# Optimization experiments

Measured on AMD Instinct MI355X. Metric: run time of the kernel, lower is better.

## Reference

```python
import jax, jax.numpy as jnp
import numpy as np

MARGIN = 0.3
EPS = 1e-6  # torch TripletMarginLoss pairwise_distance eps


def setup_inputs() -> dict:
    key = jax.random.key(0)
    k1, k2 = jax.random.split(key)
    n, d = 8192, 128
    inputs = jax.random.normal(k1, (n, d), dtype=jnp.float32)
    similarity = jax.random.randint(k2, (n, n), 0, 2, dtype=jnp.int32)
    return {"inputs": inputs, "similarity": similarity}


def reference(inputs, similarity):
    # mask[i, j] = True if j is a positive of anchor i
    mask = similarity != 0                      # (n, n) bool
    maskf = mask.astype(inputs.dtype)
    counts = maskf.sum(axis=1, keepdims=True)   # (n, 1), >0 by construction
    # per-anchor center = mean of its positives (masked mean as a GEMM)
    centers = (maskf @ inputs) / counts         # (n, d)
    # dist[i, j] = ||centers[i] - inputs[j]||_2 via the expansion trick
    # (avoids materializing the (n, n, d) difference tensor of the original)
    c2 = jnp.sum(centers * centers, axis=1)[:, None]
    x2 = jnp.sum(inputs * inputs, axis=1)[None, :]
    d2 = c2 + x2 - 2.0 * (centers @ inputs.T)
    dist = jnp.sqrt(jnp.maximum(d2, 0.0))       # (n, n)
    # dist only feeds argmin in the original (indices carry no grad)
    dist = jax.lax.stop_gradient(dist)
    # hard-negative mining: argmin of dist over negatives of each anchor
    neg_idx = jnp.argmin(jnp.where(mask, jnp.inf, dist), axis=1)  # (n,)
    neg_min = inputs[neg_idx]                   # (n, d)
    # TripletMarginLoss(margin=0.3, p=2): anchor=centers, pos=inputs, neg=neg_min
    d_ap = jnp.linalg.norm(centers - inputs + EPS, axis=1)
    d_an = jnp.linalg.norm(centers - neg_min + EPS, axis=1)
    return jnp.mean(jnp.maximum(d_ap - d_an + MARGIN, 0.0))
```

## Files before the change

kernel.cpp:

```cpp
#include <hip/hip_runtime.h>
#include <stdint.h>

#define NN 8192
#define DD 128

typedef float f32x4 __attribute__((ext_vector_type(4)));
typedef short bf16x8 __attribute__((ext_vector_type(8)));

union B8 { uint32_t u[4]; bf16x8 v; };

__device__ inline uint16_t f2bf(float f) {
  uint32_t u = __builtin_bit_cast(uint32_t, f);
  uint32_t r = (u + 0x7FFFu + ((u >> 16) & 1u)) >> 16;
  return (uint16_t)r;
}

__device__ inline f32x4 mfma16(bf16x8 a, bf16x8 b, f32x4 c) {
  return __builtin_amdgcn_mfma_f32_16x16x32_bf16(a, b, c, 0, 0, 0);
}

__global__ __launch_bounds__(256) void k_prep(const float* __restrict__ inp,
                                              uint16_t* __restrict__ inp_bf,
                                              uint16_t* __restrict__ inpT_bf,
                                              float* __restrict__ x2p,
                                              uint32_t* __restrict__ counts,
                                              uint32_t* __restrict__ negkey,
                                              float* __restrict__ out) {
  __shared__ uint16_t ldsT[128 * 65];
  __shared__ float ldsS[256];
  const int tid = threadIdx.x;
  const int gid = blockIdx.x * 256 + tid;
  if (gid < NN) { counts[gid] = 0u; negkey[gid] = 0xFFFFFFFFu; }
  if (gid == 0) out[0] = 0.f;
  const int j0 = blockIdx.x * 64;
  const int r = tid >> 2;
  const int dseg = (tid & 3) * 32;
  float ss = 0.f;
#pragma unroll
  for (int it = 0; it < 8; ++it) {
    float4 v = *(const float4*)(inp + (size_t)(j0 + r) * DD + dseg + it * 4);
    ss += v.x * v.x + v.y * v.y + v.z * v.z + v.w * v.w;
    uint16_t b0 = f2bf(v.x), b1 = f2bf(v.y), b2 = f2bf(v.z), b3 = f2bf(v.w);
    *(ushort4*)(inp_bf + (size_t)(j0 + r) * DD + dseg + it * 4) = make_ushort4(b0, b1, b2, b3);
    int d = dseg + it * 4;
    ldsT[(d + 0) * 65 + r] = b0;
    ldsT[(d + 1) * 65 + r] = b1;
    ldsT[(d + 2) * 65 + r] = b2;
    ldsT[(d + 3) * 65 + r] = b3;
  }
  ldsS[tid] = ss;
  __syncthreads();
  if (tid < 64)
    x2p[j0 + tid] = ldsS[tid * 4] + ldsS[tid * 4 + 1] + ldsS[tid * 4 + 2] + ldsS[tid * 4 + 3] + 512.0f;
#pragma unroll
  for (int it = 0; it < 32; ++it) {
    int flat = it * 256 + tid;
    int d = flat >> 6, jl = flat & 63;
    inpT_bf[(size_t)d * NN + j0 + jl] = ldsT[d * 65 + jl];
  }
}

__global__ __launch_bounds__(256, 2) void k_bitgen(const int* __restrict__ sim,
                                                   uint32_t* __restrict__ bmT,
                                                   uint32_t* __restrict__ counts) {
  __shared__ uint32_t ldsW[64 * 64];
  const int tid = threadIdx.x, lane = tid & 63, w = tid >> 6;
  const int m0 = blockIdx.x * 64;
  const int c0 = blockIdx.y * 2048;
  int va[32], vb[32];
  {
    const int* p = sim + (size_t)(m0 + w) * NN + c0 + lane;
#pragma unroll
    for (int s = 0; s < 32; ++s) va[s] = p[s * 64];
  }
#pragma unroll 1
  for (int rr = 0; rr < 16; ++rr) {
    const int rl = rr * 4 + w;
    if (rr < 15) {
      const int* p = sim + (size_t)(m0 + rl + 4) * NN + c0 + lane;
#pragma unroll
      for (int s = 0; s < 32; ++s) vb[s] = p[s * 64];
    }
    uint32_t cnt = 0;
#pragma unroll
    for (int s = 0; s < 32; ++s) {
      unsigned long long ball = __ballot(va[s] != 0);
      cnt += (uint32_t)__popcll(ball);
      if ((lane & 31) == 0)
        ldsW[(s * 2 + (lane >> 5)) * 64 + rl] = (uint32_t)(ball >> (lane & 32));
    }
    if (lane == 0) atomicAdd(&counts[m0 + rl], cnt);
#pragma unroll
    for (int s = 0; s < 32; ++s) va[s] = vb[s];
  }
  __syncthreads();
#pragma unroll
  for (int it = 0; it < 16; ++it) {
    int idx = it * 256 + tid;
    int kw = idx >> 6, r = idx & 63;
    bmT[(size_t)((c0 >> 5) + kw) * NN + m0 + r] = ldsW[idx];
  }
}

__global__ __launch_bounds__(256, 4) void k_gemm1(const uint16_t* __restrict__ inpT,
                                                  const uint32_t* __restrict__ bmT,
                                                  float* __restrict__ part) {
  __shared__ __align__(16) uint16_t ldsB[128 * 72];
  __shared__ uint32_t ldsM[128];
  const int tid = threadIdx.x, lane = tid & 63, w = tid >> 6;
  const int col = lane & 15, quad = lane >> 4;
  const int m0 = blockIdx.x * 64;
  const int kb0 = blockIdx.y * 1024;
  const int wm = (w >> 1) * 32, wn = (w & 1) * 64;
  const int dim = tid >> 1, koff = (tid & 1) * 32;
  const int mrow = tid >> 1, msel = tid & 1;
  f32x4 acc[2][4];
  const f32x4 z = {0.f, 0.f, 0.f, 0.f};
#pragma unroll
  for (int r = 0; r < 2; ++r)
#pragma unroll
    for (int c = 0; c < 4; ++c) acc[r][c] = z;

  bf16x8 bpf[4];
#pragma unroll
  for (int it = 0; it < 4; ++it)
    bpf[it] = *(const bf16x8*)(inpT + (size_t)dim * NN + kb0 + koff + it * 8);
  uint32_t mpf = (tid < 128) ? bmT[(size_t)((kb0 >> 5) + msel) * NN + m0 + mrow] : 0u;

  for (int ks = 0; ks < 16; ++ks) {
    const int kb = kb0 + ks * 64;
    __syncthreads();
#pragma unroll
    for (int it = 0; it < 4; ++it)
      *(bf16x8*)(ldsB + dim * 72 + koff + it * 8) = bpf[it];
    if (tid < 128) ldsM[mrow * 2 + msel] = mpf;
    __syncthreads();
    if (ks < 15) {
#pragma unroll
      for (int it = 0; it < 4; ++it)
        bpf[it] = *(const bf16x8*)(inpT + (size_t)dim * NN + kb + 64 + koff + it * 8);
      if (tid < 128) mpf = bmT[(size_t)(((kb + 64) >> 5) + msel) * NN + m0 + mrow];
    }
#pragma unroll
    for (int h = 0; h < 2; ++h) {
      B8 af[2];
#pragma unroll
      for (int rr = 0; rr < 2; ++rr) {
        uint32_t word = ldsM[(wm + rr * 16 + col) * 2 + h];
        uint32_t b = (word >> (quad * 8)) & 0xFFu;
        uint32_t s = b * 0x8001u;
#pragma unroll
        for (int p = 0; p < 4; ++p) {
          uint32_t t = (s >> (2 * p)) & 0x10001u;
          af[rr].u[p] = t * 0x3F80u;
        }
      }
#pragma unroll
      for (int cc = 0; cc < 4; ++cc) {
        bf16x8 bfr = *(const bf16x8*)(ldsB + (wn + cc * 16 + col) * 72 + h * 32 + quad * 8);
#pragma unroll
        for (int rr = 0; rr < 2; ++rr) acc[rr][cc] = mfma16(af[rr].v, bfr, acc[rr][cc]);
      }
    }
  }
  float* pp = part + (size_t)blockIdx.y * NN * DD;
#pragma unroll
  for (int rr = 0; rr < 2; ++rr)
#pragma unroll
    for (int cc = 0; cc < 4; ++cc)
#pragma unroll
      for (int g = 0; g < 4; ++g)
        pp[(size_t)(m0 + wm + rr * 16 + quad * 4 + g) * DD + wn + cc * 16 + col] = acc[rr][cc][g];
}

__global__ __launch_bounds__(256) void k_reduce(const float* __restrict__ part,
                                                const uint32_t* __restrict__ counts,
                                                float* __restrict__ centers,
                                                uint16_t* __restrict__ cen_bf) {
  const int gid = blockIdx.x * 256 + threadIdx.x;
  const int idx = gid * 4;
  const int row = idx >> 7;
  const float inv = 1.0f / (float)counts[row];
  float4 v = *(const float4*)(part + idx);
#pragma unroll
  for (int s = 1; s < 8; ++s) {
    float4 u = *(const float4*)(part + (size_t)s * NN * DD + idx);
    v.x += u.x; v.y += u.y; v.z += u.z; v.w += u.w;
  }
  v.x *= inv; v.y *= inv; v.z *= inv; v.w *= inv;
  *(float4*)(centers + idx) = v;
  *(ushort4*)(cen_bf + idx) = make_ushort4(f2bf(v.x), f2bf(v.y), f2bf(v.z), f2bf(v.w));
}

__global__ __launch_bounds__(256, 4) void k_argmin(const uint16_t* __restrict__ cen_bf,
                                                   const uint16_t* __restrict__ inp_bf,
                                                   const uint32_t* __restrict__ bmT,
                                                   const float* __restrict__ x2p,
                                                   uint32_t* __restrict__ negkey) {
  __shared__ __align__(16) uint16_t ldsB[64 * 136];
  __shared__ uint32_t ldsM[128];
  __shared__ float ldsX[64];
  __shared__ uint32_t ldsR[64];
  const int tid = threadIdx.x, lane = tid & 63, w = tid >> 6;
  const int col = lane & 15, quad = lane >> 4;
  const int i0 = blockIdx.x * 64;
  const int jbase = blockIdx.y * 1024;
  const int wi = (w >> 1) * 32, wj = (w & 1) * 32;
  bf16x8 af[2][4];
#pragma unroll
  for (int rr = 0; rr < 2; ++rr)
#pragma unroll
    for (int kk = 0; kk < 4; ++kk)
      af[rr][kk] = *(const bf16x8*)(cen_bf + (size_t)(i0 + wi + rr * 16 + col) * DD + kk * 32 + quad * 8);
  if (tid < 64) ldsR[tid] = 0xFFFFFFFFu;
  uint32_t best[2][4];
#pragma unroll
  for (int rr = 0; rr < 2; ++rr)
#pragma unroll
    for (int g = 0; g < 4; ++g) best[rr][g] = 0xFFFFFFFFu;

  const int jl = tid >> 2, doff = (tid & 3) * 32;
  bf16x8 bpf[4];
#pragma unroll
  for (int it = 0; it < 4; ++it)
    bpf[it] = *(const bf16x8*)(inp_bf + (size_t)(jbase + jl) * DD + doff + it * 8);
  uint32_t mpf = (tid < 128) ? bmT[(size_t)((jbase >> 5) + (tid >> 6)) * NN + i0 + (tid & 63)] : 0u;
  float xpf = (tid >= 128 && tid < 192) ? x2p[jbase + tid - 128] : 0.f;

  for (int js = 0; js < 16; ++js) {
    const int j0 = jbase + js * 64;
    __syncthreads();
#pragma unroll
    for (int it = 0; it < 4; ++it)
      *(bf16x8*)(ldsB + jl * 136 + doff + it * 8) = bpf[it];
    if (tid < 128) ldsM[tid] = mpf;
    else if (tid < 192) ldsX[tid - 128] = xpf;
    __syncthreads();
    if (js < 15) {
#pragma unroll
      for (int it = 0; it < 4; ++it)
        bpf[it] = *(const bf16x8*)(inp_bf + (size_t)(j0 + 64 + jl) * DD + doff + it * 8);
      if (tid < 128) mpf = bmT[(size_t)(((j0 + 64) >> 5) + (tid >> 6)) * NN + i0 + (tid & 63)];
      else if (tid < 192) xpf = x2p[j0 + 64 + tid - 128];
    }
    f32x4 acc[2][2];
    const f32x4 z = {0.f, 0.f, 0.f, 0.f};
    acc[0][0] = z; acc[0][1] = z; acc[1][0] = z; acc[1][1] = z;
#pragma unroll
    for (int kk = 0; kk < 4; ++kk) {
      bf16x8 b0 = *(const bf16x8*)(ldsB + (wj + col) * 136 + kk * 32 + quad * 8);
      bf16x8 b1 = *(const bf16x8*)(ldsB + (wj + 16 + col) * 136 + kk * 32 + quad * 8);
      acc[0][0] = mfma16(af[0][kk], b0, acc[0][0]);
      acc[0][1] = mfma16(af[0][kk], b1, acc[0][1]);
      acc[1][0] = mfma16(af[1][kk], b0, acc[1][0]);
      acc[1][1] = mfma16(af[1][kk], b1, acc[1][1]);
    }
    const uint32_t wsel = (w & 1) * 64;
    uint32_t words[2][4];
#pragma unroll
    for (int rr = 0; rr < 2; ++rr)
#pragma unroll
      for (int g = 0; g < 4; ++g) words[rr][g] = ldsM[wsel + wi + rr * 16 + quad * 4 + g];
#pragma unroll
    for (int cc = 0; cc < 2; ++cc) {
      const int jj = wj + cc * 16 + col;
      const float xq = ldsX[jj];
      const uint32_t jpre = (uint32_t)(j0 + jj);
      const int sh = 31 - (cc * 16 + col);
#pragma unroll
      for (int rr = 0; rr < 2; ++rr)
#pragma unroll
        for (int g = 0; g < 4; ++g) {
          float v = fmaf(-2.0f, acc[rr][cc][g], xq);
          uint32_t u = __builtin_bit_cast(uint32_t, v);
          uint32_t key = (u & 0xFFFFE000u) | jpre;
          key |= (words[rr][g] << sh) & 0x80000000u;
          best[rr][g] = min(best[rr][g], key);
        }
    }
  }
#pragma unroll
  for (int rr = 0; rr < 2; ++rr)
#pragma unroll
    for (int g = 0; g < 4; ++g) {
      uint32_t k = best[rr][g];
#pragma unroll
      for (int d = 1; d < 16; d <<= 1) {
        uint32_t o = (uint32_t)__shfl_xor((int)k, d);
        k = min(k, o);
      }
      if (col == 0) atomicMin(&ldsR[wi + rr * 16 + quad * 4 + g], k);
    }
  __syncthreads();
  if (tid < 64) atomicMin(&negkey[i0 + tid], ldsR[tid]);
}

__global__ __launch_bounds__(256) void k_loss(const float* __restrict__ centers,
                                              const float* __restrict__ inp,
                                              const uint32_t* __restrict__ negkey,
                                              float* __restrict__ out) {
  __shared__ float lds[4];
  const int tid = threadIdx.x, lane = tid & 63, w = tid >> 6;
  float local = 0.f;
#pragma unroll 1
  for (int a = 0; a < 4; ++a) {
    int i = blockIdx.x * 16 + w * 4 + a;
    float2 c = *(const float2*)(centers + (size_t)i * DD + lane * 2);
    float2 x = *(const float2*)(inp + (size_t)i * DD + lane * 2);
    uint32_t ni = negkey[i] & (NN - 1);
    float2 gv = *(const float2*)(inp + (size_t)ni * DD + lane * 2);
    float e0 = c.x - x.x + 1e-6f, e1 = c.y - x.y + 1e-6f;
    float f0 = c.x - gv.x + 1e-6f, f1 = c.y - gv.y + 1e-6f;
    float dap = e0 * e0 + e1 * e1;
    float dan = f0 * f0 + f1 * f1;
#pragma unroll
    for (int d = 32; d; d >>= 1) {
      dap += __shfl_down(dap, d);
      dan += __shfl_down(dan, d);
    }
    if (lane == 0) local += fmaxf(sqrtf(dap) - sqrtf(dan) + 0.3f, 0.f);
  }
  if (lane == 0) lds[w] = local;
  __syncthreads();
  if (tid == 0) atomicAdd(out, (lds[0] + lds[1] + lds[2] + lds[3]) * (1.0f / 8192.0f));
}

extern "C" void kernel_launch(void* const* d_in, const int* in_sizes, int n_in,
                              void* d_out, int out_size, void* d_ws, size_t ws_size,
                              hipStream_t stream) {
  (void)in_sizes; (void)n_in; (void)out_size; (void)ws_size;
  const float* inp = (const float*)d_in[0];
  const int* sim = (const int*)d_in[1];
  float* out = (float*)d_out;
  char* ws = (char*)d_ws;

  uint32_t* bmT     = (uint32_t*)ws;
  float* part       = (float*)(ws + (8u << 20));
  float* centers    = (float*)(ws + (40u << 20));
  uint16_t* inp_bf  = (uint16_t*)(ws + (44u << 20));
  uint16_t* inpT_bf = (uint16_t*)(ws + (46u << 20));
  uint16_t* cen_bf  = (uint16_t*)(ws + (48u << 20));
  float* x2p        = (float*)(ws + (50u << 20));
  uint32_t* counts  = (uint32_t*)(ws + (50u << 20) + 32768u);
  uint32_t* negkey  = (uint32_t*)(ws + (50u << 20) + 65536u);

  k_prep<<<128, 256, 0, stream>>>(inp, inp_bf, inpT_bf, x2p, counts, negkey, out);
  k_bitgen<<<dim3(128, 4), 256, 0, stream>>>(sim, bmT, counts);
  k_gemm1<<<dim3(128, 8), 256, 0, stream>>>(inpT_bf, bmT, part);
  k_reduce<<<1024, 256, 0, stream>>>(part, counts, centers, cen_bf);
  k_argmin<<<dim3(128, 8), 256, 0, stream>>>(cen_bf, inp_bf, bmT, x2p, negkey);
  k_loss<<<512, 256, 0, stream>>>(centers, inp, negkey, out);
}
```

Measured before the change: 446.7 us.

## Fuse prep with bitgen and fold split-K reduce into gemm1 via tickets

Merges the input prep and bitmask generation kernels into one launch by splitting blocks by index. The split-K reduction is folded into gemm1: the last block for each row tile, found through an atomic ticket counter, sums the partials and writes the centers. Per-chunk counts are written directly instead of atomically accumulated. This removes two kernel launches and their inter-kernel gaps. In exchange, the final reduce for each tile runs on a single block, which serialises the tail.

```diff
diff --git a/kernel.cpp b/kernel.cpp
--- a/kernel.cpp
+++ b/kernel.cpp
@@ -19,54 +19,60 @@
   return __builtin_amdgcn_mfma_f32_16x16x32_bf16(a, b, c, 0, 0, 0);
 }
 
-__global__ __launch_bounds__(256) void k_prep(const float* __restrict__ inp,
-                                              uint16_t* __restrict__ inp_bf,
-                                              uint16_t* __restrict__ inpT_bf,
-                                              float* __restrict__ x2p,
-                                              uint32_t* __restrict__ counts,
-                                              uint32_t* __restrict__ negkey,
-                                              float* __restrict__ out) {
+__global__ __launch_bounds__(256, 2) void k_prepbit(const float* __restrict__ inp,
+                                                    const int* __restrict__ sim,
+                                                    uint16_t* __restrict__ inp_bf,
+                                                    uint16_t* __restrict__ inpT_bf,
+                                                    float* __restrict__ x2p,
+                                                    uint32_t* __restrict__ bmT,
+                                                    uint32_t* __restrict__ counts4,
+                                                    uint32_t* __restrict__ negkey,
+                                                    uint32_t* __restrict__ tickets,
+                                                    float* __restrict__ out) {
   __shared__ uint16_t ldsT[128 * 65];
   __shared__ float ldsS[256];
-  const int tid = threadIdx.x;
-  const int gid = blockIdx.x * 256 + tid;
-  if (gid < NN) { counts[gid] = 0u; negkey[gid] = 0xFFFFFFFFu; }
-  if (gid == 0) out[0] = 0.f;
-  const int j0 = blockIdx.x * 64;
-  const int r = tid >> 2;
-  const int dseg = (tid & 3) * 32;
-  float ss = 0.f;
-#pragma unroll
-  for (int it = 0; it < 8; ++it) {
-    float4 v = *(const float4*)(inp + (size_t)(j0 + r) * DD + dseg + it * 4);
-    ss += v.x * v.x + v.y * v.y + v.z * v.z + v.w * v.w;
-    uint16_t b0 = f2bf(v.x), b1 = f2bf(v.y), b2 = f2bf(v.z), b3 = f2bf(v.w);
-    *(ushort4*)(inp_bf + (size_t)(j0 + r) * DD + dseg + it * 4) = make_ushort4(b0, b1, b2, b3);
-    int d = dseg + it * 4;
-    ldsT[(d + 0) * 65 + r] = b0;
-    ldsT[(d + 1) * 65 + r] = b1;
-    ldsT[(d + 2) * 65 + r] = b2;
-    ldsT[(d + 3) * 65 + r] = b3;
-  }
-  ldsS[tid] = ss;
-  __syncthreads();
-  if (tid < 64)
-    x2p[j0 + tid] = ldsS[tid * 4] + ldsS[tid * 4 + 1] + ldsS[tid * 4 + 2] + ldsS[tid * 4 + 3] + 512.0f;
-#pragma unroll
-  for (int it = 0; it < 32; ++it) {
-    int flat = it * 256 + tid;
-    int d = flat >> 6, jl = flat & 63;
-    inpT_bf[(size_t)d * NN + j0 + jl] = ldsT[d * 65 + jl];
-  }
-}
-
-__global__ __launch_bounds__(256, 2) void k_bitgen(const int* __restrict__ sim,
-                                                   uint32_t* __restrict__ bmT,
-                                                   uint32_t* __restrict__ counts) {
   __shared__ uint32_t ldsW[64 * 64];
   const int tid = threadIdx.x, lane = tid & 63, w = tid >> 6;
-  const int m0 = blockIdx.x * 64;
-  const int c0 = blockIdx.y * 2048;
+
+  if (blockIdx.x < 128) {
+    const int px = blockIdx.x;
+    const int gid = px * 256 + tid;
+    if (gid < NN) negkey[gid] = 0xFFFFFFFFu;
+    if (px == 0 && tid < 128) tickets[tid] = 0u;
+    if (gid == 0) out[0] = 0.f;
+    const int j0 = px * 64;
+    const int r = tid >> 2;
+    const int dseg = (tid & 3) * 32;
+    float ss = 0.f;
+#pragma unroll
+    for (int it = 0; it < 8; ++it) {
+      float4 v = *(const float4*)(inp + (size_t)(j0 + r) * DD + dseg + it * 4);
+      ss += v.x * v.x + v.y * v.y + v.z * v.z + v.w * v.w;
+      uint16_t b0 = f2bf(v.x), b1 = f2bf(v.y), b2 = f2bf(v.z), b3 = f2bf(v.w);
+      *(ushort4*)(inp_bf + (size_t)(j0 + r) * DD + dseg + it * 4) = make_ushort4(b0, b1, b2, b3);
+      int d = dseg + it * 4;
+      ldsT[(d + 0) * 65 + r] = b0;
+      ldsT[(d + 1) * 65 + r] = b1;
+      ldsT[(d + 2) * 65 + r] = b2;
+      ldsT[(d + 3) * 65 + r] = b3;
+    }
+    ldsS[tid] = ss;
+    __syncthreads();
+    if (tid < 64)
+      x2p[j0 + tid] = ldsS[tid * 4] + ldsS[tid * 4 + 1] + ldsS[tid * 4 + 2] + ldsS[tid * 4 + 3] + 512.0f;
+#pragma unroll
+    for (int it = 0; it < 32; ++it) {
+      int flat = it * 256 + tid;
+      int d = flat >> 6, jl = flat & 63;
+      inpT_bf[(size_t)d * NN + j0 + jl] = ldsT[d * 65 + jl];
+    }
+    return;
+  }
+
+  const int bx = blockIdx.x - 128;
+  const int m0 = (bx & 127) * 64;
+  const int cy = bx >> 7;
+  const int c0 = cy * 2048;
   int va[32], vb[32];
   {
     const int* p = sim + (size_t)(m0 + w) * NN + c0 + lane;
@@ -89,7 +95,7 @@
       if ((lane & 31) == 0)
         ldsW[(s * 2 + (lane >> 5)) * 64 + rl] = (uint32_t)(ball >> (lane & 32));
     }
-    if (lane == 0) atomicAdd(&counts[m0 + rl], cnt);
+    if (lane == 0) counts4[(size_t)cy * NN + m0 + rl] = cnt;
 #pragma unroll
     for (int s = 0; s < 32; ++s) va[s] = vb[s];
   }
@@ -104,9 +110,14 @@
 
 __global__ __launch_bounds__(256, 4) void k_gemm1(const uint16_t* __restrict__ inpT,
                                                   const uint32_t* __restrict__ bmT,
-                                                  float* __restrict__ part) {
+                                                  float* __restrict__ part,
+                                                  const uint32_t* __restrict__ counts4,
+                                                  uint32_t* __restrict__ tickets,
+                                                  float* __restrict__ centers,
+                                                  uint16_t* __restrict__ cen_bf) {
   __shared__ __align__(16) uint16_t ldsB[128 * 72];
   __shared__ uint32_t ldsM[128];
+  __shared__ int lastFlag;
   const int tid = threadIdx.x, lane = tid & 63, w = tid >> 6;
   const int col = lane & 15, quad = lane >> 4;
   const int m0 = blockIdx.x * 64;
@@ -171,25 +182,33 @@
 #pragma unroll
       for (int g = 0; g < 4; ++g)
         pp[(size_t)(m0 + wm + rr * 16 + quad * 4 + g) * DD + wn + cc * 16 + col] = acc[rr][cc][g];
-}
-
-__global__ __launch_bounds__(256) void k_reduce(const float* __restrict__ part,
-                                                const uint32_t* __restrict__ counts,
-                                                float* __restrict__ centers,
-                                                uint16_t* __restrict__ cen_bf) {
-  const int gid = blockIdx.x * 256 + threadIdx.x;
-  const int idx = gid * 4;
-  const int row = idx >> 7;
-  const float inv = 1.0f / (float)counts[row];
-  float4 v = *(const float4*)(part + idx);
-#pragma unroll
-  for (int s = 1; s < 8; ++s) {
-    float4 u = *(const float4*)(part + (size_t)s * NN * DD + idx);
-    v.x += u.x; v.y += u.y; v.z += u.z; v.w += u.w;
-  }
-  v.x *= inv; v.y *= inv; v.z *= inv; v.w *= inv;
-  *(float4*)(centers + idx) = v;
-  *(ushort4*)(cen_bf + idx) = make_ushort4(f2bf(v.x), f2bf(v.y), f2bf(v.z), f2bf(v.w));
+
+  __syncthreads();
+  if (tid == 0) {
+    __threadfence();
+    lastFlag = (atomicAdd(&tickets[blockIdx.x], 1u) == 7u) ? 1 : 0;
+  }
+  __syncthreads();
+  if (!lastFlag) return;
+  __threadfence();
+  const int base = m0 * DD;
+#pragma unroll 1
+  for (int r8 = 0; r8 < 8; ++r8) {
+    const int li = r8 * 1024 + tid * 4;
+    const int fidx = base + li;
+    const int row = m0 + (li >> 7);
+    const float inv = 1.0f / (float)(counts4[row] + counts4[NN + row] +
+                                     counts4[2 * NN + row] + counts4[3 * NN + row]);
+    float4 v = *(const float4*)(part + fidx);
+#pragma unroll
+    for (int s = 1; s < 8; ++s) {
+      float4 u = *(const float4*)(part + (size_t)s * NN * DD + fidx);
+      v.x += u.x; v.y += u.y; v.z += u.z; v.w += u.w;
+    }
+    v.x *= inv; v.y *= inv; v.z *= inv; v.w *= inv;
+    *(float4*)(centers + fidx) = v;
+    *(ushort4*)(cen_bf + fidx) = make_ushort4(f2bf(v.x), f2bf(v.y), f2bf(v.z), f2bf(v.w));
+  }
 }
 
 __global__ __launch_bounds__(256, 4) void k_argmin(const uint16_t* __restrict__ cen_bf,
@@ -341,13 +360,14 @@
   uint16_t* inpT_bf = (uint16_t*)(ws + (46u << 20));
   uint16_t* cen_bf  = (uint16_t*)(ws + (48u << 20));
   float* x2p        = (float*)(ws + (50u << 20));
-  uint32_t* counts  = (uint32_t*)(ws + (50u << 20) + 32768u);
-  uint32_t* negkey  = (uint32_t*)(ws + (50u << 20) + 65536u);
-
-  k_prep<<<128, 256, 0, stream>>>(inp, inp_bf, inpT_bf, x2p, counts, negkey, out);
-  k_bitgen<<<dim3(128, 4), 256, 0, stream>>>(sim, bmT, counts);
-  k_gemm1<<<dim3(128, 8), 256, 0, stream>>>(inpT_bf, bmT, part);
-  k_reduce<<<1024, 256, 0, stream>>>(part, counts, centers, cen_bf);
+  uint32_t* counts4 = (uint32_t*)(ws + (50u << 20) + 32768u);
+  uint32_t* negkey  = (uint32_t*)(ws + (50u << 20) + 163840u);
+  uint32_t* tickets = (uint32_t*)(ws + (50u << 20) + 196608u);
+
+  k_prepbit<<<640, 256, 0, stream>>>(inp, sim, inp_bf, inpT_bf, x2p, bmT, counts4,
+                                     negkey, tickets, out);
+  k_gemm1<<<dim3(128, 8), 256, 0, stream>>>(inpT_bf, bmT, part, counts4, tickets,
+                                            centers, cen_bf);
   k_argmin<<<dim3(128, 8), 256, 0, stream>>>(cen_bf, inp_bf, bmT, x2p, negkey);
   k_loss<<<512, 256, 0, stream>>>(centers, inp, negkey, out);
 }
```

Result: slower. 491.5 us (+10.0%).
